# Kernel optimization log

Measured on AMD Instinct MI355X. Metric: run time of the kernel, lower is better.

Reference implementation:

```python
import jax, jax.numpy as jnp
import numpy as np

BIG = 1000000.0
EPS = 1e-06
COST_CLASS, COST_BBOX, COST_GIOU = 1.0, 5.0, 2.0


def sanitize_boxes(boxes):
    # boxes: [..., 4] cxcywh
    boxes = jnp.nan_to_num(boxes, nan=0.0, posinf=1.0, neginf=0.0)
    cx, cy, w, h = jnp.moveaxis(boxes, -1, 0)
    cx = jnp.clip(cx, 0.0, 1.0)
    cy = jnp.clip(cy, 0.0, 1.0)
    w = jnp.clip(w, EPS, 1.0)
    h = jnp.clip(h, EPS, 1.0)
    return jnp.stack([cx, cy, w, h], axis=-1)


def box_cxcywh_to_xyxy(x):
    cx, cy, w, h = jnp.moveaxis(x, -1, 0)
    return jnp.stack([cx - 0.5 * w, cy - 0.5 * h, cx + 0.5 * w, cy + 0.5 * h], axis=-1)


def pairwise_giou(b1, b2):
    # b1: [B, Q, 4] xyxy, b2: [B, T, 4] xyxy -> [B, Q, T]
    area1 = (b1[..., 2] - b1[..., 0]) * (b1[..., 3] - b1[..., 1])  # [B,Q]
    area2 = (b2[..., 2] - b2[..., 0]) * (b2[..., 3] - b2[..., 1])  # [B,T]
    lt = jnp.maximum(b1[:, :, None, :2], b2[:, None, :, :2])  # [B,Q,T,2]
    rb = jnp.minimum(b1[:, :, None, 2:], b2[:, None, :, 2:])
    wh = jnp.clip(rb - lt, 0.0)
    inter = wh[..., 0] * wh[..., 1]  # [B,Q,T]
    union = area1[:, :, None] + area2[:, None, :] - inter
    iou = inter / union
    # enclosing box
    lt_c = jnp.minimum(b1[:, :, None, :2], b2[:, None, :, :2])
    rb_c = jnp.maximum(b1[:, :, None, 2:], b2[:, None, :, 2:])
    wh_c = jnp.clip(rb_c - lt_c, 0.0)
    area_c = wh_c[..., 0] * wh_c[..., 1]
    return iou - (area_c - union) / area_c


def reference(pred_logits, pred_boxes, tgt_labels, tgt_boxes):
    # Batched cost-matrix construction of HungarianMatcher.forward.
    out_logits = jnp.nan_to_num(pred_logits, nan=0.0, posinf=0.0, neginf=0.0)
    out_prob = jax.nn.softmax(out_logits, axis=-1)  # [B,Q,C]
    out_bbox = sanitize_boxes(pred_boxes)           # [B,Q,4]
    t_bbox = sanitize_boxes(tgt_boxes)              # [B,T,4]

    # cost_class[b,q,t] = -out_prob[b,q,tgt_labels[b,t]]
    B, Q, C = out_prob.shape
    T = tgt_labels.shape[1]
    gather_idx = jnp.broadcast_to(tgt_labels[:, None, :], (B, Q, T))
    cost_class = -jnp.take_along_axis(out_prob, gather_idx, axis=2)  # [B,Q,T]

    # L1 cdist in cxcywh space
    cost_bbox = jnp.sum(jnp.abs(out_bbox[:, :, None, :] - t_bbox[:, None, :, :]), axis=-1)

    cost_giou = -pairwise_giou(box_cxcywh_to_xyxy(out_bbox), box_cxcywh_to_xyxy(t_bbox))

    Cmat = COST_CLASS * cost_class + COST_BBOX * cost_bbox + COST_GIOU * cost_giou
    return jnp.nan_to_num(Cmat, nan=BIG, posinf=BIG, neginf=BIG)


def setup_inputs() -> dict:
    key = jax.random.key(0)
    k1, k2, k3, k4 = jax.random.split(key, 4)
    B, Q, C, T = 64, 900, 256, 200
    return {
        "pred_logits": jax.random.normal(k1, (B, Q, C), dtype=jnp.float32),
        "pred_boxes": jax.random.uniform(k2, (B, Q, 4), dtype=jnp.float32),
        "tgt_labels": jax.random.randint(k3, (B, T), 0, C),
        "tgt_boxes": jax.random.uniform(k4, (B, T, 4), dtype=jnp.float32),
    }
```

## Files before the change

kernel.cpp:

```cpp
#include <hip/hip_runtime.h>
#include <math.h>

constexpr int B = 64, Q = 900, C = 256, T = 200;
constexpr float EPSV = 1e-6f;
constexpr int WPB = 4;
constexpr int QPW = 2;
constexpr int QPB = WPB * QPW;
constexpr int NT4 = T / 4;

__device__ __forceinline__ float clampf(float x, float lo, float hi) {
    return fminf(fmaxf(x, lo), hi);
}

__global__ __launch_bounds__(256, 8)
void matcher_kernel(const float* __restrict__ logits,
                    const float* __restrict__ pboxes,
                    const int*   __restrict__ tlabels,
                    const float* __restrict__ tboxes,
                    float* __restrict__ out)
{
    __shared__ float s_exp[WPB][C][2];

    const int blocks_per_b = (Q + QPB - 1) / QPB;
    const int b    = blockIdx.x / blocks_per_b;
    const int qblk = blockIdx.x % blocks_per_b;
    const int wave = threadIdx.x >> 6;
    const int lane = threadIdx.x & 63;
    const int q0   = qblk * QPB + wave * QPW;
    if (q0 >= Q) return;

    const bool act = lane < NT4;
    float tx0[4], ty0[4], tx1[4], ty1[4], twd[4], tht[4];
    int   lidx[4];
    {
        const float* tb_base = tboxes + b * (T * 4);
        const int*   tl_base = tlabels + b * T;
        const int t0i = act ? 4 * lane : 0;
        #pragma unroll
        for (int s = 0; s < 4; ++s) {
            int t = t0i + s;
            float4 tb = ((const float4*)tb_base)[t];
            float cx = clampf(tb.x, 0.0f, 1.0f);
            float cy = clampf(tb.y, 0.0f, 1.0f);
            float w  = clampf(tb.z, EPSV, 1.0f);
            float h  = clampf(tb.w, EPSV, 1.0f);
            twd[s] = w;  tht[s] = h;
            tx0[s] = cx - 0.5f * w;  ty0[s] = cy - 0.5f * h;
            tx1[s] = cx + 0.5f * w;  ty1[s] = cy + 0.5f * h;
            lidx[s] = min(max(tl_base[t], 0), C - 1);
        }
    }

    const size_t rowa = (size_t)b * Q + q0;
    const size_t rowb = rowa + 1;

    const float4 lga = ((const float4*)(logits + rowa * C))[lane];
    const float4 lgb = ((const float4*)(logits + rowb * C))[lane];
    const float4 pba = *(const float4*)(pboxes + rowa * 4);
    const float4 pbb = *(const float4*)(pboxes + rowb * 4);

    float ea0 = __expf(lga.x), ea1 = __expf(lga.y);
    float ea2 = __expf(lga.z), ea3 = __expf(lga.w);
    float eb0 = __expf(lgb.x), eb1 = __expf(lgb.y);
    float eb2 = __expf(lgb.z), eb3 = __expf(lgb.w);
    float sa = (ea0 + ea1) + (ea2 + ea3);
    float sb = (eb0 + eb1) + (eb2 + eb3);
    #pragma unroll
    for (int off = 32; off; off >>= 1) {
        sa += __shfl_xor(sa, off);
        sb += __shfl_xor(sb, off);
    }
    const float inva = __builtin_amdgcn_rcpf(sa);
    const float invb = __builtin_amdgcn_rcpf(sb);

    float* dst = &s_exp[wave][4 * lane][0];
    ((float4*)dst)[0] = make_float4(ea0, eb0, ea1, eb1);
    ((float4*)dst)[1] = make_float4(ea2, eb2, ea3, eb3);

    float pcxa = clampf(pba.x, 0.0f, 1.0f), pcya = clampf(pba.y, 0.0f, 1.0f);
    float pwa  = clampf(pba.z, EPSV, 1.0f), pha  = clampf(pba.w, EPSV, 1.0f);
    float pax0 = pcxa - 0.5f * pwa, pay0 = pcya - 0.5f * pha;
    float pax1 = pcxa + 0.5f * pwa, pay1 = pcya + 0.5f * pha;
    float psxa = pax0 + pax1, psya = pay0 + pay1;
    float pareaa = pwa * pha;

    float pcxb = clampf(pbb.x, 0.0f, 1.0f), pcyb = clampf(pbb.y, 0.0f, 1.0f);
    float pwb  = clampf(pbb.z, EPSV, 1.0f), phb  = clampf(pbb.w, EPSV, 1.0f);
    float pbx0 = pcxb - 0.5f * pwb, pby0 = pcyb - 0.5f * phb;
    float pbx1 = pcxb + 0.5f * pwb, pby1 = pcyb + 0.5f * phb;
    float psxb = pbx0 + pbx1, psyb = pby0 + pby1;
    float pareab = pwb * phb;

    float resa[4], resb[4];
    #pragma unroll
    for (int s = 0; s < 4; ++s) {
        const float* g2 = &s_exp[wave][lidx[s]][0];
        const float ga = g2[0], gb = g2[1];
        const float tsx = tx0[s] + tx1[s];
        const float tsy = ty0[s] + ty1[s];
        const float tarea = twd[s] * tht[s];

        {
            float t0 = fmaf(-ga, inva, 2.0f);
            float s1 = fabsf(psxa - tsx) + fabsf(psya - tsy);
            float s2 = fabsf(pwa - twd[s]) + fabsf(pha - tht[s]);
            float iw = fmaxf(fminf(pax1, tx1[s]) - fmaxf(pax0, tx0[s]), 0.0f);
            float ih = fmaxf(fminf(pay1, ty1[s]) - fmaxf(pay0, ty0[s]), 0.0f);
            float inter = iw * ih;
            float uni = pareaa + tarea - inter;
            float cw = fmaxf(pax1, tx1[s]) - fminf(pax0, tx0[s]);
            float ch = fmaxf(pay1, ty1[s]) - fminf(pay0, ty0[s]);
            float ca = cw * ch;
            float num = fmaf(uni, uni, inter * ca);
            float val = num * __builtin_amdgcn_rcpf(uni * ca);
            float cost = fmaf(2.5f, s1, t0);
            cost = fmaf(5.0f, s2, cost);
            resa[s] = fmaf(-2.0f, val, cost);
        }
        {
            float t0 = fmaf(-gb, invb, 2.0f);
            float s1 = fabsf(psxb - tsx) + fabsf(psyb - tsy);
            float s2 = fabsf(pwb - twd[s]) + fabsf(phb - tht[s]);
            float iw = fmaxf(fminf(pbx1, tx1[s]) - fmaxf(pbx0, tx0[s]), 0.0f);
            float ih = fmaxf(fminf(pby1, ty1[s]) - fmaxf(pby0, ty0[s]), 0.0f);
            float inter = iw * ih;
            float uni = pareab + tarea - inter;
            float cw = fmaxf(pbx1, tx1[s]) - fminf(pbx0, tx0[s]);
            float ch = fmaxf(pby1, ty1[s]) - fminf(pby0, ty0[s]);
            float ca = cw * ch;
            float num = fmaf(uni, uni, inter * ca);
            float val = num * __builtin_amdgcn_rcpf(uni * ca);
            float cost = fmaf(2.5f, s1, t0);
            cost = fmaf(5.0f, s2, cost);
            resb[s] = fmaf(-2.0f, val, cost);
        }
    }

    if (act) {
        float4* oa = (float4*)(out + rowa * T);
        float4* ob = (float4*)(out + rowb * T);
        oa[lane] = make_float4(resa[0], resa[1], resa[2], resa[3]);
        ob[lane] = make_float4(resb[0], resb[1], resb[2], resb[3]);
    }
}

extern "C" void kernel_launch(void* const* d_in, const int* in_sizes, int n_in,
                              void* d_out, int out_size, void* d_ws, size_t ws_size,
                              hipStream_t stream) {
    const float* logits  = (const float*)d_in[0];
    const float* pboxes  = (const float*)d_in[1];
    const int*   tlabels = (const int*)d_in[2];
    const float* tboxes  = (const float*)d_in[3];
    float* out = (float*)d_out;

    const int blocks_per_b = (Q + QPB - 1) / QPB;
    dim3 grid(B * blocks_per_b);
    dim3 block(64 * WPB);
    matcher_kernel<<<grid, block, 0, stream>>>(logits, pboxes, tlabels, tboxes, out);
}
```

Measured before the change: 113.4 us.

## Use DPP wave reduction, vectorize target loads, simplify enclosing-box math

The softmax denominator reduction changes from shfl_xor butterflies to DPP row shifts plus row broadcasts, then reads lane 63. Target box and label loads are reordered after the logits loads, and the labels are fetched as one int4. The enclosing-box width and height are now derived algebraically as the sum of widths minus the raw intersection, which drops the separate min/max operations. The kernel is likely memory-bound on logits reads and output writes, so these ALU savings may matter little.

```diff
diff --git a/kernel.cpp b/kernel.cpp
--- a/kernel.cpp
+++ b/kernel.cpp
@@ -11,6 +11,10 @@
 __device__ __forceinline__ float clampf(float x, float lo, float hi) {
     return fminf(fmaxf(x, lo), hi);
 }
+
+#define DPP_ADD_STEP(x, ctrl, row_mask)                                        \
+    (x) += __int_as_float(__builtin_amdgcn_update_dpp(                         \
+        0, __float_as_int(x), (ctrl), (row_mask), 0xf, true))
 
 __global__ __launch_bounds__(256, 8)
 void matcher_kernel(const float* __restrict__ logits,
@@ -29,28 +33,6 @@
     const int q0   = qblk * QPB + wave * QPW;
     if (q0 >= Q) return;
 
-    const bool act = lane < NT4;
-    float tx0[4], ty0[4], tx1[4], ty1[4], twd[4], tht[4];
-    int   lidx[4];
-    {
-        const float* tb_base = tboxes + b * (T * 4);
-        const int*   tl_base = tlabels + b * T;
-        const int t0i = act ? 4 * lane : 0;
-        #pragma unroll
-        for (int s = 0; s < 4; ++s) {
-            int t = t0i + s;
-            float4 tb = ((const float4*)tb_base)[t];
-            float cx = clampf(tb.x, 0.0f, 1.0f);
-            float cy = clampf(tb.y, 0.0f, 1.0f);
-            float w  = clampf(tb.z, EPSV, 1.0f);
-            float h  = clampf(tb.w, EPSV, 1.0f);
-            twd[s] = w;  tht[s] = h;
-            tx0[s] = cx - 0.5f * w;  ty0[s] = cy - 0.5f * h;
-            tx1[s] = cx + 0.5f * w;  ty1[s] = cy + 0.5f * h;
-            lidx[s] = min(max(tl_base[t], 0), C - 1);
-        }
-    }
-
     const size_t rowa = (size_t)b * Q + q0;
     const size_t rowb = rowa + 1;
 
@@ -59,19 +41,46 @@
     const float4 pba = *(const float4*)(pboxes + rowa * 4);
     const float4 pbb = *(const float4*)(pboxes + rowb * 4);
 
+    const bool act = lane < NT4;
+    const int  t0i = act ? 4 * lane : 0;
+    const float4* tb_base = (const float4*)(tboxes + b * (T * 4));
+    const float4 tbr[4] = {tb_base[t0i], tb_base[t0i + 1],
+                           tb_base[t0i + 2], tb_base[t0i + 3]};
+    const int4 labs = *(const int4*)(tlabels + b * T + t0i);
+
+    float tx0[4], ty0[4], tx1[4], ty1[4], twd[4], tht[4];
+    int   lidx[4];
+    {
+        const int lbs[4] = {labs.x, labs.y, labs.z, labs.w};
+        #pragma unroll
+        for (int s = 0; s < 4; ++s) {
+            float cx = clampf(tbr[s].x, 0.0f, 1.0f);
+            float cy = clampf(tbr[s].y, 0.0f, 1.0f);
+            float w  = clampf(tbr[s].z, EPSV, 1.0f);
+            float h  = clampf(tbr[s].w, EPSV, 1.0f);
+            twd[s] = w;  tht[s] = h;
+            tx0[s] = cx - 0.5f * w;  ty0[s] = cy - 0.5f * h;
+            tx1[s] = cx + 0.5f * w;  ty1[s] = cy + 0.5f * h;
+            lidx[s] = min(max(lbs[s], 0), C - 1);
+        }
+    }
+
     float ea0 = __expf(lga.x), ea1 = __expf(lga.y);
     float ea2 = __expf(lga.z), ea3 = __expf(lga.w);
     float eb0 = __expf(lgb.x), eb1 = __expf(lgb.y);
     float eb2 = __expf(lgb.z), eb3 = __expf(lgb.w);
     float sa = (ea0 + ea1) + (ea2 + ea3);
     float sb = (eb0 + eb1) + (eb2 + eb3);
-    #pragma unroll
-    for (int off = 32; off; off >>= 1) {
-        sa += __shfl_xor(sa, off);
-        sb += __shfl_xor(sb, off);
-    }
-    const float inva = __builtin_amdgcn_rcpf(sa);
-    const float invb = __builtin_amdgcn_rcpf(sb);
+    DPP_ADD_STEP(sa, 0x111, 0xf);  DPP_ADD_STEP(sb, 0x111, 0xf);
+    DPP_ADD_STEP(sa, 0x112, 0xf);  DPP_ADD_STEP(sb, 0x112, 0xf);
+    DPP_ADD_STEP(sa, 0x114, 0xf);  DPP_ADD_STEP(sb, 0x114, 0xf);
+    DPP_ADD_STEP(sa, 0x118, 0xf);  DPP_ADD_STEP(sb, 0x118, 0xf);
+    DPP_ADD_STEP(sa, 0x142, 0xa);  DPP_ADD_STEP(sb, 0x142, 0xa);
+    DPP_ADD_STEP(sa, 0x143, 0xc);  DPP_ADD_STEP(sb, 0x143, 0xc);
+    const float inva = __builtin_amdgcn_rcpf(__int_as_float(
+        __builtin_amdgcn_readlane(__float_as_int(sa), 63)));
+    const float invb = __builtin_amdgcn_rcpf(__int_as_float(
+        __builtin_amdgcn_readlane(__float_as_int(sb), 63)));
 
     float* dst = &s_exp[wave][4 * lane][0];
     ((float4*)dst)[0] = make_float4(ea0, eb0, ea1, eb1);
@@ -104,12 +113,12 @@
             float t0 = fmaf(-ga, inva, 2.0f);
             float s1 = fabsf(psxa - tsx) + fabsf(psya - tsy);
             float s2 = fabsf(pwa - twd[s]) + fabsf(pha - tht[s]);
-            float iw = fmaxf(fminf(pax1, tx1[s]) - fmaxf(pax0, tx0[s]), 0.0f);
-            float ih = fmaxf(fminf(pay1, ty1[s]) - fmaxf(pay0, ty0[s]), 0.0f);
-            float inter = iw * ih;
-            float uni = pareaa + tarea - inter;
-            float cw = fmaxf(pax1, tx1[s]) - fminf(pax0, tx0[s]);
-            float ch = fmaxf(pay1, ty1[s]) - fminf(pay0, ty0[s]);
+            float iwr = fminf(pax1, tx1[s]) - fmaxf(pax0, tx0[s]);
+            float ihr = fminf(pay1, ty1[s]) - fmaxf(pay0, ty0[s]);
+            float inter = fmaxf(iwr, 0.0f) * fmaxf(ihr, 0.0f);
+            float uni = fmaf(twd[s], tht[s], pareaa) - inter;
+            float cw = (pwa + twd[s]) - iwr;
+            float ch = (pha + tht[s]) - ihr;
             float ca = cw * ch;
             float num = fmaf(uni, uni, inter * ca);
             float val = num * __builtin_amdgcn_rcpf(uni * ca);
@@ -121,12 +130,12 @@
             float t0 = fmaf(-gb, invb, 2.0f);
             float s1 = fabsf(psxb - tsx) + fabsf(psyb - tsy);
             float s2 = fabsf(pwb - twd[s]) + fabsf(phb - tht[s]);
-            float iw = fmaxf(fminf(pbx1, tx1[s]) - fmaxf(pbx0, tx0[s]), 0.0f);
-            float ih = fmaxf(fminf(pby1, ty1[s]) - fmaxf(pby0, ty0[s]), 0.0f);
-            float inter = iw * ih;
-            float uni = pareab + tarea - inter;
-            float cw = fmaxf(pbx1, tx1[s]) - fminf(pbx0, tx0[s]);
-            float ch = fmaxf(pby1, ty1[s]) - fminf(pby0, ty0[s]);
+            float iwr = fminf(pbx1, tx1[s]) - fmaxf(pbx0, tx0[s]);
+            float ihr = fminf(pby1, ty1[s]) - fmaxf(pby0, ty0[s]);
+            float inter = fmaxf(iwr, 0.0f) * fmaxf(ihr, 0.0f);
+            float uni = fmaf(twd[s], tht[s], pareab) - inter;
+            float cw = (pwb + twd[s]) - iwr;
+            float ch = (phb + tht[s]) - ihr;
             float ca = cw * ch;
             float num = fmaf(uni, uni, inter * ca);
             float val = num * __builtin_amdgcn_rcpf(uni * ca);
```

New measurement: 112.2 us. No clear change (-1.0%).
